# Performance work log

Measured on AMD Instinct MI355X. Metric: run time of the kernel, lower is better.

Reference implementation:

```python
import jax, jax.numpy as jnp
import numpy as np
from jax import lax

C = 128        # args.feat_dim
HF = WF = 320  # feature map spatial size
IMG = 1280     # segmentation map resolution
N = 256        # number of anchors
CROP = 32      # fixed crop size (h and w)
NUM_CLASSES = 151
NUM_BASE = 64


def setup_inputs() -> dict:
    key = jax.random.key(0)
    ks = jax.random.split(key, 9)
    feature_map = jax.random.normal(ks[0], (C, HF, WF), dtype=jnp.float32)
    seg = jax.random.randint(ks[1], (IMG, IMG), 0, NUM_CLASSES, dtype=jnp.int32)
    x0 = jax.random.randint(ks[2], (N,), 0, WF - CROP, dtype=jnp.int32)
    y0 = jax.random.randint(ks[3], (N,), 0, HF - CROP, dtype=jnp.int32)
    # anchors layout matches torch code: [x0, x1, y0, y1] in feature-map pixels
    anchors = jnp.stack([x0, x0 + CROP, y0, y0 + CROP], axis=1)
    labels = jax.random.randint(ks[4], (N,), 0, NUM_BASE, dtype=jnp.int32)
    base_classes = jax.random.randint(ks[5], (NUM_BASE,), 0, NUM_CLASSES, dtype=jnp.int32)
    W1 = jax.random.normal(ks[6], (256, C, 3, 3), dtype=jnp.float32) * 0.02
    b1 = jnp.zeros((256,), dtype=jnp.float32)
    W2 = jax.random.normal(ks[7], (1, 256, 3, 3), dtype=jnp.float32) * 0.02
    b2 = jnp.zeros((1,), dtype=jnp.float32)
    return {"feature_map": feature_map, "seg": seg, "anchors": anchors,
            "labels": labels, "base_classes": base_classes,
            "W1": W1, "b1": b1, "W2": W2, "b2": b2}


def reference(feature_map, seg, anchors, labels, base_classes, W1, b1, W2, b2):
    # F.interpolate(mode='nearest') from IMGxIMG down to HFxWF: idx = floor(i * in/out)
    hi = (jnp.arange(HF) * seg.shape[0]) // HF
    wi = (jnp.arange(WF) * seg.shape[1]) // WF
    mask = seg[hi][:, wi].astype(jnp.float32)  # [HF, WF]

    starts = anchors[:, jnp.array([2, 0])]  # (h0, w0) per anchor

    def crop_feat(s):
        return lax.dynamic_slice(feature_map, (jnp.int32(0), s[0], s[1]), (C, CROP, CROP))

    def crop_mask(s):
        return lax.dynamic_slice(mask, (s[0], s[1]), (CROP, CROP))

    crops = jax.vmap(crop_feat)(starts)       # [N, C, CROP, CROP]
    mask_crops = jax.vmap(crop_mask)(starts)  # [N, CROP, CROP]

    dn = ('NCHW', 'OIHW', 'NCHW')
    h = lax.conv_general_dilated(crops, W1, (1, 1), 'SAME', dimension_numbers=dn)
    h = jax.nn.relu(h + b1[None, :, None, None])
    logits = lax.conv_general_dilated(h, W2, (1, 1), 'SAME', dimension_numbers=dn)
    logits = logits + b2[None, :, None, None]  # [N, 1, CROP, CROP]

    tgt_cls = base_classes[labels].astype(jnp.float32)  # [N]
    tgt = (mask_crops == tgt_cls[:, None, None]).astype(jnp.float32)[:, None]  # [N,1,CROP,CROP]

    # stable BCE-with-logits: max(x,0) - x*t + log1p(exp(-|x|))
    bce = jnp.maximum(logits, 0.0) - logits * tgt + jnp.log1p(jnp.exp(-jnp.abs(logits)))
    per_anchor = bce.mean(axis=(1, 2, 3))  # mean per anchor, as in F.binary_cross_entropy_with_logits
    return per_anchor.sum() / (N + 1e-10)
```

## Files before the change

kernel.cpp:

```cpp
#include <hip/hip_runtime.h>

typedef __attribute__((ext_vector_type(8))) short short8;
typedef __attribute__((ext_vector_type(8))) int int8v;
typedef __attribute__((ext_vector_type(16))) float floatx16;
typedef __attribute__((ext_vector_type(4))) unsigned int uint4v;
typedef unsigned short ushort_t;
typedef unsigned int uint_t;
typedef unsigned char uchar_t;

#define NA   256
#define CIN  128
#define HFD  320
#define FMPX (HFD*HFD)
#define IMGD 1280

#define W1R_BYTE_OFF (1u<<20)
#define W2R_BYTE_OFF ((1u<<20) + 9*256*128)
#define FMT_BYTE_OFF (2u<<20)

#define SAPL_Q 5440
#define PSTR_Q 4112

union V32 { int8v v; uint4v q[2]; };

__device__ __forceinline__ ushort_t f2bf(float v) {
    uint_t u = __float_as_uint(v);
    return (ushort_t)((u + 0x8000u) >> 16);
}
__device__ __forceinline__ uchar_t f2fp8(float v) {
    int r = __builtin_amdgcn_cvt_pk_fp8_f32(v, 0.0f, 0, false);
    return (uchar_t)(r & 0xff);
}

__global__ __launch_bounds__(256) void prep_misc(
    const float* __restrict__ W1, const float* __restrict__ W2,
    float* __restrict__ logits, float* __restrict__ out,
    uchar_t* __restrict__ w1b, ushort_t* __restrict__ w2r)
{
    const int b = blockIdx.x, t = threadIdx.x;
    if (b < 1024) {
        logits[b * 256 + t] = 0.0f;
    } else if (b < 1024 + 128) {
        int e = (b - 1024) * 256 + t;
        int oc = e >> 7, cin = e & 127;
        int g = oc >> 6, nt = (oc >> 5) & 1, lv = oc & 31;
        int c = cin >> 6, kh = (cin >> 5) & 1, j = cin & 31;
        #pragma unroll
        for (int tap = 0; tap < 9; ++tap) {
            int idx = (((((tap * 4 + g) * 2 + nt) * 2 + c) * 64) + kh * 32 + lv) * 32 + j;
            w1b[idx] = f2fp8(W1[(oc * 128 + cin) * 9 + tap] * 64.0f);
        }
    } else {
        #pragma unroll
        for (int i = 0; i < 32; ++i) {
            int e = i * 256 + t;
            int nrow = e >> 8, oc = e & 255;
            w2r[nrow * 256 + oc] = f2bf(nrow < 9 ? W2[oc * 9 + nrow] : 0.0f);
        }
        if (t == 0) out[0] = 0.0f;
    }
}

__global__ __launch_bounds__(256) void prep_transpose(
    const float* __restrict__ fm, uchar_t* __restrict__ fmT)
{
    __shared__ uchar_t s[32 * 144];
    const int t = threadIdx.x;
    const int y = blockIdx.y, x0b = blockIdx.x * 32;
    #pragma unroll
    for (int i = 0; i < 16; ++i) {
        int e = t + 256 * i;
        int c = e >> 5, xo = e & 31;
        s[xo * 144 + c] = f2fp8(fm[(size_t)c * FMPX + y * HFD + x0b + xo]);
    }
    __syncthreads();
    {
        int xo = t >> 3, cg = t & 7;
        uint4v v = *(const uint4v*)&s[xo * 144 + cg * 16];
        *(uint4v*)&fmT[((size_t)(y * HFD + x0b + xo)) * 128 + cg * 16] = v;
    }
}

__global__ __launch_bounds__(256, 3) void conv_mfma_kernel(
    const int* __restrict__ anchors, const uchar_t* __restrict__ fmT,
    const uchar_t* __restrict__ w1b, const ushort_t* __restrict__ w2r,
    const float* __restrict__ b1, float* __restrict__ logits)
{
    const int id   = blockIdx.x;
    const int xcd  = id & 7, sid = id >> 3;
    const int n    = xcd * 32 + (sid >> 4);
    const int rem  = sid & 15;
    const int q    = rem >> 2;
    const int g    = rem & 3;

    const int t    = threadIdx.x;
    const int w    = t >> 6;
    const int lane = t & 63;
    const int l31  = lane & 31;
    const int kh   = lane >> 5;

    const int x0 = anchors[n * 4 + 0];
    const int y0 = anchors[n * 4 + 2];
    const int r0 = q * 8;

    __shared__ __align__(16) char smem[8 * PSTR_Q];
    char* s_a = smem;

    if (t < 80) {
        int sub = t & 3, k = t >> 2;
        int pr = k >> 1, col = (k & 1) * 33;
        uint4v z = {0u, 0u, 0u, 0u};
        *(uint4v*)(s_a + sub * SAPL_Q + (pr * 34 + col) * 16) = z;
    }

    floatx16 acc[2][2];
    #pragma unroll
    for (int mt = 0; mt < 2; ++mt)
        #pragma unroll
        for (int nt = 0; nt < 2; ++nt)
            #pragma unroll
            for (int r = 0; r < 16; ++r) acc[mt][nt][r] = 0.0f;

    auto loadB = [&](int tap, int cc, V32* b) {
        #pragma unroll
        for (int nt = 0; nt < 2; ++nt) {
            const uchar_t* bp = w1b + ((((tap * 4 + g) * 2 + nt) * 2 + cc) << 11) + lane * 32;
            b[nt].q[0] = *(const uint4v*)(bp);
            b[nt].q[1] = *(const uint4v*)(bp + 16);
        }
    };

    V32 bcur[2], bnxt[2];
    loadB(0, 0, bcur);

    for (int c = 0; c < 2; ++c) {
        __syncthreads();
        #pragma unroll
        for (int j = 0; j < 5; ++j) {
            int u = t + 256 * j;
            int pr = u >> 7, rr = u & 127;
            int cell = rr >> 2, sub = rr & 3;
            int cr = r0 + pr - 1;
            uint4v v = {0u, 0u, 0u, 0u};
            if ((unsigned)cr < 32u)
                v = *(const uint4v*)&fmT[((size_t)((y0 + cr) * HFD + x0 + cell)) * 128 + c * 64 + sub * 16];
            *(uint4v*)(s_a + sub * SAPL_Q + (pr * 34 + cell + 1) * 16) = v;
        }
        __syncthreads();
        #pragma unroll 1
        for (int s = 0; s < 9; ++s) {
            const int kx = s / 3, ky = s - 3 * kx;
            {
                int s2 = s + 1;
                if (s2 < 9)      loadB((s2 - (s2 / 3) * 3) * 3 + s2 / 3, c, bnxt);
                else if (c == 0) loadB(0, 1, bnxt);
            }
            V32 a2[2];
            #pragma unroll
            for (int f = 0; f < 2; ++f) {
                int cell = (2 * w + ky + f) * 34 + l31 + kx;
                a2[f].q[0] = *(const uint4v*)(s_a + (2 * kh)     * SAPL_Q + cell * 16);
                a2[f].q[1] = *(const uint4v*)(s_a + (2 * kh + 1) * SAPL_Q + cell * 16);
            }
            #pragma unroll
            for (int mt = 0; mt < 2; ++mt) {
                acc[mt][0] = __builtin_amdgcn_mfma_scale_f32_32x32x64_f8f6f4(
                    a2[mt].v, bcur[0].v, acc[mt][0], 0, 0, 0, 127, 0, 127);
                acc[mt][1] = __builtin_amdgcn_mfma_scale_f32_32x32x64_f8f6f4(
                    a2[mt].v, bcur[1].v, acc[mt][1], 0, 0, 0, 127, 0, 127);
            }
            bcur[0] = bnxt[0];
            bcur[1] = bnxt[1];
        }
    }

    __syncthreads();
    #pragma unroll
    for (int nt = 0; nt < 2; ++nt) {
        float bias = b1[g * 64 + nt * 32 + l31];
        int plane = nt * 4 + (l31 >> 3);
        #pragma unroll
        for (int mt = 0; mt < 2; ++mt) {
            int lr = 2 * w + mt;
            #pragma unroll
            for (int reg = 0; reg < 16; ++reg) {
                int col = (reg & 3) + 8 * (reg >> 2) + 4 * kh;
                float hv = fmaxf(fmaf(acc[mt][nt][reg], 0.015625f, bias), 0.0f);
                *(ushort_t*)(smem + plane * PSTR_Q + ((lr * 32 + col) * 8 + (l31 & 7)) * 2) = f2bf(hv);
            }
        }
    }
    __syncthreads();

    floatx16 vacc[2];
    #pragma unroll
    for (int mt = 0; mt < 2; ++mt)
        #pragma unroll
        for (int r = 0; r < 16; ++r) vacc[mt][r] = 0.0f;
    #pragma unroll
    for (int ks = 0; ks < 4; ++ks) {
        short8 bw = *(const short8*)&w2r[l31 * 256 + g * 64 + ks * 16 + kh * 8];
        #pragma unroll
        for (int mt = 0; mt < 2; ++mt) {
            short8 ah = *(const short8*)(smem + (ks * 2 + kh) * PSTR_Q + ((2 * w + mt) * 32 + l31) * 16);
            vacc[mt] = __builtin_amdgcn_mfma_f32_32x32x16_bf16(ah, bw, vacc[mt], 0, 0, 0);
        }
    }

    __syncthreads();
    float* s_log = (float*)smem;
    for (int i = t; i < 320; i += 256) s_log[i] = 0.0f;
    __syncthreads();
    if (l31 < 9) {
        int ky = l31 / 3, kx = l31 - ky * 3;
        #pragma unroll
        for (int mt = 0; mt < 2; ++mt) {
            int outr = 2 * w + mt + 2 - ky;
            #pragma unroll
            for (int reg = 0; reg < 16; ++reg) {
                int col  = (reg & 3) + 8 * (reg >> 2) + 4 * kh;
                int outc = col + 1 - kx;
                if (outc >= 0 && outc < 32)
                    atomicAdd(&s_log[outr * 32 + outc], vacc[mt][reg]);
            }
        }
    }
    __syncthreads();
    for (int i = t; i < 320; i += 256) {
        int outr = i >> 5, outc = i & 31;
        int R = r0 + outr - 1;
        if ((unsigned)R < 32u)
            atomicAdd(&logits[n * 1024 + R * 32 + outc], s_log[i]);
    }
}

__global__ __launch_bounds__(256) void bce_reduce_kernel(
    const float* __restrict__ logits, const int* __restrict__ seg,
    const int* __restrict__ anchors, const int* __restrict__ labels,
    const int* __restrict__ base_classes, const float* __restrict__ b2,
    float* __restrict__ out)
{
    const int n = blockIdx.x;
    const int t = threadIdx.x;
    const int y0 = anchors[n * 4 + 2];
    const int x0 = anchors[n * 4 + 0];
    const int tgt_cls = base_classes[labels[n]];
    const float bias2 = b2[0];

    float lsum = 0.0f;
    #pragma unroll
    for (int r = 0; r < 4; ++r) {
        int p = t + r * 256;
        int i = p >> 5, j = p & 31;
        float l = logits[n * 1024 + p] + bias2;
        int sv = seg[(size_t)(4 * (y0 + i)) * IMGD + 4 * (x0 + j)];
        float tgt = (sv == tgt_cls) ? 1.0f : 0.0f;
        lsum += fmaxf(l, 0.0f) - l * tgt + log1pf(expf(-fabsf(l)));
    }
    #pragma unroll
    for (int off = 32; off > 0; off >>= 1) lsum += __shfl_down(lsum, off, 64);
    __shared__ float s[4];
    if ((t & 63) == 0) s[t >> 6] = lsum;
    __syncthreads();
    if (t == 0) {
        float tot = s[0] + s[1] + s[2] + s[3];
        const float scale = 1.0f / (1024.0f * (256.0f + 1e-10f));
        atomicAdd(out, tot * scale);
    }
}

extern "C" void kernel_launch(void* const* d_in, const int* in_sizes, int n_in,
                              void* d_out, int out_size, void* d_ws, size_t ws_size,
                              hipStream_t stream) {
    const float* fm           = (const float*)d_in[0];
    const int*   seg          = (const int*)d_in[1];
    const int*   anchors      = (const int*)d_in[2];
    const int*   labels       = (const int*)d_in[3];
    const int*   base_classes = (const int*)d_in[4];
    const float* W1           = (const float*)d_in[5];
    const float* b1           = (const float*)d_in[6];
    const float* W2           = (const float*)d_in[7];
    const float* b2           = (const float*)d_in[8];
    float* out = (float*)d_out;

    float*    logits = (float*)d_ws;
    uchar_t*  w1b    = (uchar_t*)((char*)d_ws + W1R_BYTE_OFF);
    ushort_t* w2r    = (ushort_t*)((char*)d_ws + W2R_BYTE_OFF);
    uchar_t*  fmT    = (uchar_t*)((char*)d_ws + FMT_BYTE_OFF);

    prep_misc<<<1024 + 128 + 1, 256, 0, stream>>>(W1, W2, logits, out, w1b, w2r);
    prep_transpose<<<dim3(10, 320), 256, 0, stream>>>(fm, fmT);
    conv_mfma_kernel<<<4096, 256, 0, stream>>>(anchors, fmT, w1b, w2r, b1, logits);
    bce_reduce_kernel<<<NA, 256, 0, stream>>>(logits, seg, anchors, labels, base_classes, b2, out);
}
```

Measured before the change: 231.6 us.

## Stage both channel halves at once and triple-buffer weight loads

The two per-half channel passes become a single staging of all 128 input channels into LDS (8 planes), which removes two barriers and the second global fill. The 18 MFMA steps now run in an unrolled loop that keeps three rotating weight register buffers, so weight fetches are issued two steps ahead. s_log gets its own shared array, which drops one barrier. The cost is more LDS per block (about 44KB against about 33KB) and more registers, which may lower occupancy.

Result: slower. 654.0 us (+182.4%).

```diff
diff --git a/kernel.cpp b/kernel.cpp
--- a/kernel.cpp
+++ b/kernel.cpp
@@ -18,7 +18,7 @@
 #define W2R_BYTE_OFF ((1u<<20) + 9*256*128)
 #define FMT_BYTE_OFF (2u<<20)
 
-#define SAPL_Q 5440
+#define SAPL_M 5456
 #define PSTR_Q 4112
 
 union V32 { int8v v; uint4v q[2]; };
@@ -103,15 +103,9 @@
     const int y0 = anchors[n * 4 + 2];
     const int r0 = q * 8;
 
-    __shared__ __align__(16) char smem[8 * PSTR_Q];
+    __shared__ __align__(16) char smem[8 * SAPL_M];
+    __shared__ float s_log[10 * 32];
     char* s_a = smem;
-
-    if (t < 80) {
-        int sub = t & 3, k = t >> 2;
-        int pr = k >> 1, col = (k & 1) * 33;
-        uint4v z = {0u, 0u, 0u, 0u};
-        *(uint4v*)(s_a + sub * SAPL_Q + (pr * 34 + col) * 16) = z;
-    }
 
     floatx16 acc[2][2];
     #pragma unroll
@@ -130,49 +124,67 @@
         }
     };
 
-    V32 bcur[2], bnxt[2];
-    loadB(0, 0, bcur);
-
-    for (int c = 0; c < 2; ++c) {
-        __syncthreads();
-        #pragma unroll
-        for (int j = 0; j < 5; ++j) {
-            int u = t + 256 * j;
-            int pr = u >> 7, rr = u & 127;
-            int cell = rr >> 2, sub = rr & 3;
-            int cr = r0 + pr - 1;
-            uint4v v = {0u, 0u, 0u, 0u};
-            if ((unsigned)cr < 32u)
-                v = *(const uint4v*)&fmT[((size_t)((y0 + cr) * HFD + x0 + cell)) * 128 + c * 64 + sub * 16];
-            *(uint4v*)(s_a + sub * SAPL_Q + (pr * 34 + cell + 1) * 16) = v;
-        }
-        __syncthreads();
-        #pragma unroll 1
-        for (int s = 0; s < 9; ++s) {
-            const int kx = s / 3, ky = s - 3 * kx;
-            {
-                int s2 = s + 1;
-                if (s2 < 9)      loadB((s2 - (s2 / 3) * 3) * 3 + s2 / 3, c, bnxt);
-                else if (c == 0) loadB(0, 1, bnxt);
-            }
-            V32 a2[2];
-            #pragma unroll
-            for (int f = 0; f < 2; ++f) {
-                int cell = (2 * w + ky + f) * 34 + l31 + kx;
-                a2[f].q[0] = *(const uint4v*)(s_a + (2 * kh)     * SAPL_Q + cell * 16);
-                a2[f].q[1] = *(const uint4v*)(s_a + (2 * kh + 1) * SAPL_Q + cell * 16);
-            }
-            #pragma unroll
-            for (int mt = 0; mt < 2; ++mt) {
-                acc[mt][0] = __builtin_amdgcn_mfma_scale_f32_32x32x64_f8f6f4(
-                    a2[mt].v, bcur[0].v, acc[mt][0], 0, 0, 0, 127, 0, 127);
-                acc[mt][1] = __builtin_amdgcn_mfma_scale_f32_32x32x64_f8f6f4(
-                    a2[mt].v, bcur[1].v, acc[mt][1], 0, 0, 0, 127, 0, 127);
-            }
-            bcur[0] = bnxt[0];
-            bcur[1] = bnxt[1];
-        }
-    }
+    V32 b0[2], b1v[2], b2[2];
+    loadB(0, 0, b0);
+    loadB(3, 0, b1v);
+
+    if (t < 160) {
+        int p = t & 7, k = t >> 3;
+        int pr = k >> 1, col = (k & 1) * 33;
+        uint4v z = {0u, 0u, 0u, 0u};
+        *(uint4v*)(s_a + p * SAPL_M + (pr * 34 + col) * 16) = z;
+    }
+    #pragma unroll
+    for (int j = 0; j < 10; ++j) {
+        int u = t + 256 * j;
+        int p = u & 7, cell10 = u >> 3;
+        int pr = cell10 >> 5, colr = cell10 & 31;
+        int cr = r0 + pr - 1;
+        uint4v v = {0u, 0u, 0u, 0u};
+        if ((unsigned)cr < 32u)
+            v = *(const uint4v*)&fmT[((size_t)((y0 + cr) * HFD + x0 + colr)) * 128 + (p >> 2) * 64 + (p & 3) * 16];
+        *(uint4v*)(s_a + p * SAPL_M + (pr * 34 + colr + 1) * 16) = v;
+    }
+    __syncthreads();
+
+#define STEP(S_, BU, BP) do {                                                              \
+    const int s_ = (S_);                                                                   \
+    const int c_ = s_ / 9, r_ = s_ % 9;                                                    \
+    const int kx_ = r_ / 3, ky_ = r_ % 3;                                                  \
+    V32 a2[2];                                                                             \
+    _Pragma("unroll")                                                                      \
+    for (int f = 0; f < 2; ++f) {                                                          \
+        int cell = (2 * w + ky_ + f) * 34 + l31 + kx_;                                     \
+        a2[f].q[0] = *(const uint4v*)(s_a + (c_ * 4 + 2 * kh)     * SAPL_M + cell * 16);   \
+        a2[f].q[1] = *(const uint4v*)(s_a + (c_ * 4 + 2 * kh + 1) * SAPL_M + cell * 16);   \
+    }                                                                                      \
+    {                                                                                      \
+        int s2 = s_ + 2;                                                                   \
+        if (s2 < 18) {                                                                     \
+            int c2 = s2 / 9, r2 = s2 % 9;                                                  \
+            loadB((r2 % 3) * 3 + r2 / 3, c2, BP);                                          \
+        }                                                                                  \
+    }                                                                                      \
+    _Pragma("unroll")                                                                      \
+    for (int mt = 0; mt < 2; ++mt) {                                                       \
+        acc[mt][0] = __builtin_amdgcn_mfma_scale_f32_32x32x64_f8f6f4(                      \
+            a2[mt].v, BU[0].v, acc[mt][0], 0, 0, 0, 127, 0, 127);                          \
+        acc[mt][1] = __builtin_amdgcn_mfma_scale_f32_32x32x64_f8f6f4(                      \
+            a2[mt].v, BU[1].v, acc[mt][1], 0, 0, 0, 127, 0, 127);                          \
+    }                                                                                      \
+} while (0)
+
+    #pragma unroll 1
+    for (int gi = 0; gi < 3; ++gi) {
+        const int sb = 6 * gi;
+        STEP(sb + 0, b0,  b2);
+        STEP(sb + 1, b1v, b0);
+        STEP(sb + 2, b2,  b1v);
+        STEP(sb + 3, b0,  b2);
+        STEP(sb + 4, b1v, b0);
+        STEP(sb + 5, b2,  b1v);
+    }
+#undef STEP
 
     __syncthreads();
     #pragma unroll
@@ -207,8 +219,6 @@
         }
     }
 
-    __syncthreads();
-    float* s_log = (float*)smem;
     for (int i = t; i < 320; i += 256) s_log[i] = 0.0f;
     __syncthreads();
     if (l31 < 9) {
```
